# Kernel optimization log

Hardware: AMD Instinct MI355X
Metric: run time of the kernel (lower is better)

## Reference

```python
import jax, jax.numpy as jnp
import numpy as np

DIM = 768
H = 16
HD = DIM // H  # 48


def setup_inputs() -> dict:
    key = jax.random.key(0)
    ks = jax.random.split(key, 9)
    s = 0.02
    return {
        "x": jax.random.normal(ks[0], (8, 1024, DIM), dtype=jnp.float32),
        "w_qkv": jax.random.normal(ks[1], (3 * DIM, DIM), dtype=jnp.float32) * s,
        "b_qkv": jax.random.normal(ks[2], (3 * DIM,), dtype=jnp.float32) * s,
        "w_l": jax.random.normal(ks[3], (H, H), dtype=jnp.float32) * 0.25,
        "b_l": jax.random.normal(ks[4], (H,), dtype=jnp.float32) * s,
        "w_w": jax.random.normal(ks[5], (H, H), dtype=jnp.float32) * 0.25,
        "b_w": jax.random.normal(ks[6], (H,), dtype=jnp.float32) * s,
        "w_proj": jax.random.normal(ks[7], (DIM, DIM), dtype=jnp.float32) * s,
        "b_proj": jax.random.normal(ks[8], (DIM,), dtype=jnp.float32) * s,
    }


def reference(x, w_qkv, b_qkv, w_l, b_l, w_w, b_w, w_proj, b_proj):
    B, N, C = x.shape
    scale = HD ** -0.5
    qkv = x @ w_qkv.T + b_qkv                        # [B,N,3C]
    qkv = qkv.reshape(B, N, 3, H, HD).transpose(2, 0, 3, 1, 4)  # [3,B,H,N,HD]
    q = qkv[0] * scale
    k = qkv[1]
    v = qkv[2]
    attn = jnp.einsum('bhqd,bhkd->bhqk', q, k)       # [B,H,N,N]
    # talking-heads mix before softmax (Linear over head dim)
    attn = jnp.einsum('bhqk,gh->bgqk', attn, w_l) + b_l[None, :, None, None]
    attn = jax.nn.softmax(attn, axis=-1)
    # talking-heads mix after softmax
    attn = jnp.einsum('bhqk,gh->bgqk', attn, w_w) + b_w[None, :, None, None]
    out = jnp.einsum('bhqk,bhkd->bhqd', attn, v)     # [B,H,N,HD]
    out = out.transpose(0, 2, 1, 3).reshape(B, N, C)
    return out @ w_proj.T + b_proj
```

## Files before the change

kernel.cpp:

```cpp
#include <hip/hip_runtime.h>

typedef unsigned short u16;
typedef unsigned int u32;
using short8 = __attribute__((__ext_vector_type__(8))) short;
using f32x4  = __attribute__((__ext_vector_type__(4))) float;

#define DIM 768
#define QKV3 2304
#define SEQ 1024
#define SCALE 0.14433756729740643f

__device__ __forceinline__ u16 f2bf(float f) {
  __bf16 h = (__bf16)f;
  u16 r;
  __builtin_memcpy(&r, &h, 2);
  return r;
}
__device__ __forceinline__ u32 packbf(float lo, float hi) {
  return (u32)f2bf(lo) | ((u32)f2bf(hi) << 16);
}
__device__ __forceinline__ void store1(u16* p, float v) { *p = f2bf(v); }
__device__ __forceinline__ void store1(float* p, float v) { *p = v; }

__device__ __forceinline__ f32x4 mfma16(short8 a, short8 b, f32x4 c) {
  return __builtin_amdgcn_mfma_f32_16x16x32_bf16(a, b, c, 0, 0, 0);
}

__device__ __forceinline__ void gload16(const void* g, void* l) {
  __builtin_amdgcn_global_load_lds(
      (const __attribute__((address_space(1))) unsigned int*)g,
      (__attribute__((address_space(3))) unsigned int*)l, 16, 0, 0);
}

__global__ __launch_bounds__(256)
void cvt_f32_bf16(const float* __restrict__ src, u16* __restrict__ dst, int n8) {
  int i = blockIdx.x * 256 + threadIdx.x;
  if (i < n8) {
    float4 a = ((const float4*)src)[2 * i];
    float4 b = ((const float4*)src)[2 * i + 1];
    uint4 o = {packbf(a.x, a.y), packbf(a.z, a.w), packbf(b.x, b.y), packbf(b.z, b.w)};
    ((uint4*)dst)[i] = o;
  }
}

template <typename TO>
__global__ __launch_bounds__(256, 4)
void gemm_bb(const u16* __restrict__ A, const u16* __restrict__ W,
             const float* __restrict__ bias, TO* __restrict__ C,
             int M, int N, int K) {
  __shared__ __align__(16) u16 As[128 * 32];
  __shared__ __align__(16) u16 Bs[128 * 32];
  const int tid = threadIdx.x;
  const int lane = tid & 63;
  const int wv = tid >> 6;
  const int lq = lane & 15;
  const int lc = lane >> 4;
  const int wm = wv >> 1, wn = wv & 1;
  const int row0 = blockIdx.y * 128, col0 = blockIdx.x * 128;

  f32x4 acc[4][4];
#pragma unroll
  for (int i = 0; i < 4; ++i)
#pragma unroll
    for (int j = 0; j < 4; ++j) acc[i][j] = (f32x4){0.f, 0.f, 0.f, 0.f};

#pragma unroll 1
  for (int k0 = 0; k0 < K; k0 += 32) {
    __syncthreads();
#pragma unroll
    for (int i = 0; i < 2; ++i) {
      int c = i * 256 + tid;
      int r = c >> 2, kc = (c & 3) * 8;
      gload16(A + (size_t)(row0 + r) * K + k0 + kc, As + c * 8);
      gload16(W + (size_t)(col0 + r) * K + k0 + kc, Bs + c * 8);
    }
    __syncthreads();
    short8 af[4], bf8[4];
#pragma unroll
    for (int i = 0; i < 4; ++i)
      af[i] = *(const short8*)(As + (wm * 64 + i * 16 + lq) * 32 + lc * 8);
#pragma unroll
    for (int j = 0; j < 4; ++j)
      bf8[j] = *(const short8*)(Bs + (wn * 64 + j * 16 + lq) * 32 + lc * 8);
#pragma unroll
    for (int i = 0; i < 4; ++i)
#pragma unroll
      for (int j = 0; j < 4; ++j)
        acc[i][j] = mfma16(af[i], bf8[j], acc[i][j]);
  }
#pragma unroll
  for (int j = 0; j < 4; ++j) {
    int col = col0 + wn * 64 + j * 16 + lq;
    float bv = bias[col];
#pragma unroll
    for (int i = 0; i < 4; ++i)
#pragma unroll
      for (int r = 0; r < 4; ++r) {
        int row = row0 + wm * 64 + i * 16 + lc * 4 + r;
        store1(C + (size_t)row * N + col, acc[i][j][r] + bv);
      }
  }
}

#define KS_ELEMS 24848
#define SMEM_ELEMS 80416
#define ATTN_SMEM 160832

__global__ __launch_bounds__(512, 2)
void attn_kernel(const u16* __restrict__ qkv,
                 const float* __restrict__ wl, const float* __restrict__ bl,
                 const float* __restrict__ ww, const float* __restrict__ bw,
                 u16* __restrict__ obuf) {
  extern __shared__ __align__(16) u16 smem[];
  u16* const Ks0 = smem;
  u16* const Sb  = smem + KS_ELEMS;
  u16* const Vs  = smem + 2 * KS_ELEMS;

  const int tid = threadIdx.x;
  const int wv = tid >> 6;
  const int lane = tid & 63;
  const int lq = lane & 15;
  const int lc = lane >> 4;
  const int b = blockIdx.x >> 5;
  const int qt = blockIdx.x & 31;
  const size_t tokQ = (size_t)b * SEQ + (size_t)qt * 32;
  const size_t tokB = (size_t)b * SEQ;
  const int h0 = wv * 2;
  const short8 z8 = {0, 0, 0, 0, 0, 0, 0, 0};

  {
    u32* z = (u32*)smem;
    for (int i = tid; i < SMEM_ELEMS / 2; i += 512) z[i] = 0u;
  }

  short8 qf[2][2][2];
#pragma unroll
  for (int hh = 0; hh < 2; ++hh)
#pragma unroll
    for (int qs = 0; qs < 2; ++qs) {
      const u16* qp = qkv + (tokQ + qs * 16 + lq) * QKV3 + (h0 + hh) * 48;
      qf[hh][qs][0] = *(const short8*)(qp + lc * 8);
      short8 zq = z8;
      if (lc < 2) zq = *(const short8*)(qp + 32 + lc * 8);
      qf[hh][qs][1] = zq;
    }

  short8 wlF = z8;
  short8 wwF = z8;
  if (lc < 2) {
#pragma unroll
    for (int e = 0; e < 8; ++e) {
      wlF[e] = (short)f2bf(wl[lq * 16 + lc * 8 + e] * SCALE);
      wwF[e] = (short)f2bf(ww[lq * 16 + lc * 8 + e]);
    }
  }
  float blr[4];
#pragma unroll
  for (int r = 0; r < 4; ++r) blr[r] = bl[lc * 4 + r];
  const float bwq = bw[lq];

  short8 kpre[6], vA[3], vB[3];
  auto issueK = [&](int kt) {
#pragma unroll
    for (int t = 0; t < 6; ++t) {
      int j = t * 512 + tid;
      int kr = j / 96, cc = j - kr * 96;
      kpre[t] = *(const short8*)(qkv + (tokB + (size_t)kt * 32 + kr) * QKV3 + DIM + cc * 8);
    }
  };
  auto issueV = [&](int kt) {
#pragma unroll
    for (int t = 0; t < 3; ++t) {
      int cc = (tid >> 4) + t * 32;
      int kk = tid & 15;
      const u16* v0 = qkv + (tokB + (size_t)kt * 32 + 2 * kk) * QKV3 + 2 * DIM + cc * 8;
      vA[t] = *(const short8*)v0;
      vB[t] = *(const short8*)(v0 + QKV3);
    }
  };
  auto writeK = [&](u16* dst) {
#pragma unroll
    for (int t = 0; t < 6; ++t) {
      int j = t * 512 + tid;
      int kr = j / 96, cc = j - kr * 96;
      *(short8*)(dst + kr * 776 + cc * 8) = kpre[t];
    }
  };
  auto writeV = [&]() {
#pragma unroll
    for (int t = 0; t < 3; ++t) {
      int cc = (tid >> 4) + t * 32;
      int kk = tid & 15;
#pragma unroll
      for (int e = 0; e < 8; ++e)
        *(u32*)(Vs + (cc * 8 + e) * 40 + 2 * kk) =
            (u32)(u16)vA[t][e] | ((u32)(u16)vB[t][e] << 16);
    }
  };
  auto doQK = [&](const u16* kbase) {
#pragma unroll
    for (int ks = 0; ks < 2; ++ks) {
      short8 kf[2][2];
#pragma unroll
      for (int hh = 0; hh < 2; ++hh) {
        const u16* kb = kbase + (ks * 16 + lq) * 776 + (h0 + hh) * 48;
        kf[hh][0] = *(const short8*)(kb + lc * 8);
        short8 k1 = z8;
        if (lc < 2) k1 = *(const short8*)(kb + 32 + lc * 8);
        kf[hh][1] = k1;
      }
#pragma unroll
      for (int qs = 0; qs < 2; ++qs) {
        f32x4 s0 = {0.f, 0.f, 0.f, 0.f}, s1 = {0.f, 0.f, 0.f, 0.f};
        s0 = mfma16(qf[0][qs][0], kf[0][0], s0);
        s0 = mfma16(qf[0][qs][1], kf[0][1], s0);
        s1 = mfma16(qf[1][qs][0], kf[1][0], s1);
        s1 = mfma16(qf[1][qs][1], kf[1][1], s1);
#pragma unroll
        for (int r = 0; r < 4; ++r) {
          int q = qs * 16 + lc * 4 + r;
          int k = ks * 16 + lq;
          *(u32*)(Sb + q * 776 + k * 24 + h0) = packbf(s0[r], s1[r]);
        }
      }
    }
  };
  auto doPV = [&](f32x4 O[2][3][2]) {
#pragma unroll
    for (int hh = 0; hh < 2; ++hh) {
      const int g2 = h0 + hh;
      short8 w2f[2];
#pragma unroll
      for (int qs = 0; qs < 2; ++qs)
        w2f[qs] = *(const short8*)(Sb + (qs * 16 + lq) * 776 + g2 * 40 + lc * 8);
#pragma unroll
      for (int dt = 0; dt < 3; ++dt) {
        short8 vf = *(const short8*)(Vs + (g2 * 48 + dt * 16 + lq) * 40 + lc * 8);
#pragma unroll
        for (int qs = 0; qs < 2; ++qs)
          O[hh][dt][qs] = mfma16(w2f[qs], vf, O[hh][dt][qs]);
      }
    }
  };

  float Zac[4][4], invZ[4][4];
#pragma unroll
  for (int i = 0; i < 4; ++i)
#pragma unroll
    for (int r = 0; r < 4; ++r) Zac[i][r] = 0.f;

  f32x4 O[2][3][2];
#pragma unroll
  for (int hh = 0; hh < 2; ++hh)
#pragma unroll
    for (int dt = 0; dt < 3; ++dt)
#pragma unroll
      for (int qs = 0; qs < 2; ++qs) O[hh][dt][qs] = (f32x4){0.f, 0.f, 0.f, 0.f};

  issueK(0);
  __syncthreads();
  writeK(Ks0);
  issueK(1);
  __syncthreads();
#pragma unroll 1
  for (int kt = 0; kt < 32; ++kt) {
    u16* cur = (kt & 1) ? Vs : Ks0;
    u16* nxt = (kt & 1) ? Ks0 : Vs;
    if (kt < 31) {
      writeK(nxt);
      issueK(kt == 30 ? 0 : kt + 2);
    }
    doQK(cur);
    __syncthreads();
#pragma unroll
    for (int i = 0; i < 4; ++i) {
      const int q = wv * 4 + i;
      const u16* sq = Sb + q * 776;
#pragma unroll
      for (int ks = 0; ks < 2; ++ks) {
        short8 sf = z8;
        if (lc < 2) sf = *(const short8*)(sq + (ks * 16 + lq) * 24 + lc * 8);
        f32x4 cin = {blr[0], blr[1], blr[2], blr[3]};
        f32x4 L = mfma16(wlF, sf, cin);
#pragma unroll
        for (int r = 0; r < 4; ++r) Zac[i][r] += __expf(L[r]);
      }
    }
    __syncthreads();
  }
  issueV(0);
#pragma unroll
  for (int i = 0; i < 4; ++i)
#pragma unroll
    for (int r = 0; r < 4; ++r) {
      float z = Zac[i][r];
      z += __shfl_xor(z, 1);
      z += __shfl_xor(z, 2);
      z += __shfl_xor(z, 4);
      z += __shfl_xor(z, 8);
      invZ[i][r] = 1.0f / z;
    }

#pragma unroll 1
  for (int kt = 0; kt < 32; ++kt) {
    if (kt) doPV(O);
    writeK(Ks0);
    __syncthreads();
    writeV();
    doQK(Ks0);
    if (kt < 31) { issueK(kt + 1); issueV(kt + 1); }
    __syncthreads();
#pragma unroll
    for (int i = 0; i < 4; ++i) {
      const int q = wv * 4 + i;
      u16* const sq = Sb + q * 776;
      f32x4 L[2];
#pragma unroll
      for (int ks = 0; ks < 2; ++ks) {
        short8 sf = z8;
        if (lc < 2) sf = *(const short8*)(sq + (ks * 16 + lq) * 24 + lc * 8);
        f32x4 cin = {blr[0], blr[1], blr[2], blr[3]};
        L[ks] = mfma16(wlF, sf, cin);
      }
#pragma unroll
      for (int ks = 0; ks < 2; ++ks) {
        float p0 = __expf(L[ks][0]) * invZ[i][0];
        float p1 = __expf(L[ks][1]) * invZ[i][1];
        float p2 = __expf(L[ks][2]) * invZ[i][2];
        float p3 = __expf(L[ks][3]) * invZ[i][3];
        uint2 pv = {packbf(p0, p1), packbf(p2, p3)};
        *(uint2*)(sq + (ks * 16 + lq) * 24 + lc * 4) = pv;
      }
      f32x4 W2[2];
      f32x4 cw = {bwq, bwq, bwq, bwq};
#pragma unroll
      for (int ks = 0; ks < 2; ++ks) {
        short8 pf = z8;
        if (lc < 2) pf = *(const short8*)(sq + (ks * 16 + lq) * 24 + lc * 8);
        W2[ks] = mfma16(pf, wwF, cw);
      }
#pragma unroll
      for (int ks = 0; ks < 2; ++ks) {
        uint2 wv2 = {packbf(W2[ks][0], W2[ks][1]), packbf(W2[ks][2], W2[ks][3])};
        *(uint2*)(sq + lq * 40 + ks * 16 + lc * 4) = wv2;
      }
    }
    __syncthreads();
  }
  doPV(O);

#pragma unroll
  for (int hh = 0; hh < 2; ++hh)
#pragma unroll
    for (int dt = 0; dt < 3; ++dt)
#pragma unroll
      for (int qs = 0; qs < 2; ++qs)
#pragma unroll
        for (int r = 0; r < 4; ++r) {
          size_t row = tokQ + qs * 16 + lc * 4 + r;
          int col = (h0 + hh) * 48 + dt * 16 + lq;
          obuf[row * DIM + col] = f2bf(O[hh][dt][qs][r]);
        }
}

extern "C" void kernel_launch(void* const* d_in, const int* in_sizes, int n_in,
                              void* d_out, int out_size, void* d_ws, size_t ws_size,
                              hipStream_t stream) {
  const float* x      = (const float*)d_in[0];
  const float* w_qkv  = (const float*)d_in[1];
  const float* b_qkv  = (const float*)d_in[2];
  const float* w_l    = (const float*)d_in[3];
  const float* b_l    = (const float*)d_in[4];
  const float* w_w    = (const float*)d_in[5];
  const float* b_w    = (const float*)d_in[6];
  const float* w_proj = (const float*)d_in[7];
  const float* b_proj = (const float*)d_in[8];
  float* out = (float*)d_out;

  u16* qkv_buf  = (u16*)d_ws;
  u16* attn_buf = qkv_buf + (size_t)8192 * QKV3;
  u16* x_bf     = attn_buf;
  u16* w_qkv_bf  = (u16*)d_out;
  u16* w_proj_bf = qkv_buf;

  static int attr_done = 0;
  if (!attr_done) {
    (void)hipFuncSetAttribute(reinterpret_cast<const void*>(attn_kernel),
                              hipFuncAttributeMaxDynamicSharedMemorySize,
                              ATTN_SMEM);
    attr_done = 1;
  }

  cvt_f32_bf16<<<dim3(864), 256, 0, stream>>>(w_qkv, w_qkv_bf, 221184);
  cvt_f32_bf16<<<dim3(3072), 256, 0, stream>>>(x, x_bf, 786432);
  gemm_bb<u16><<<dim3(QKV3 / 128, 8192 / 128), 256, 0, stream>>>(
      x_bf, w_qkv_bf, b_qkv, qkv_buf, 8192, QKV3, DIM);
  attn_kernel<<<dim3(8 * 32), dim3(512), ATTN_SMEM, stream>>>(
      qkv_buf, w_l, b_l, w_w, b_w, attn_buf);
  cvt_f32_bf16<<<dim3(288), 256, 0, stream>>>(w_proj, w_proj_bf, 73728);
  gemm_bb<float><<<dim3(DIM / 128, 8192 / 128), 256, 0, stream>>>(
      attn_buf, w_proj_bf, b_proj, out, 8192, DIM, DIM);
}
```

Measured before the change: 382.4 us.

## Deepen GEMM K-tile to 64 with XOR-swizzled LDS and vectorize attention stores

The GEMM kernel now stages 64-wide K slices instead of 32, halving the number of loop iterations and barriers, and stores the tiles in LDS with an XOR swizzle to reduce bank conflicts on fragment reads. In the attention kernel, the conditional zero-masked LDS loads are replaced by unconditional loads that rely on zeroed padding or zero weight fragments. The PV MFMA operands are swapped, giving a transposed accumulator layout so the output can be written as packed 8-byte stores instead of scalar bf16 stores. The larger LDS tiles raise shared memory per block, which could lower occupancy for the GEMM.

```diff
diff --git a/kernel.cpp b/kernel.cpp
--- a/kernel.cpp
+++ b/kernel.cpp
@@ -48,8 +48,8 @@
 void gemm_bb(const u16* __restrict__ A, const u16* __restrict__ W,
              const float* __restrict__ bias, TO* __restrict__ C,
              int M, int N, int K) {
-  __shared__ __align__(16) u16 As[128 * 32];
-  __shared__ __align__(16) u16 Bs[128 * 32];
+  __shared__ __align__(16) u16 As[128 * 64];
+  __shared__ __align__(16) u16 Bs[128 * 64];
   const int tid = threadIdx.x;
   const int lane = tid & 63;
   const int wv = tid >> 6;
@@ -65,28 +65,36 @@
     for (int j = 0; j < 4; ++j) acc[i][j] = (f32x4){0.f, 0.f, 0.f, 0.f};
 
 #pragma unroll 1
-  for (int k0 = 0; k0 < K; k0 += 32) {
-    __syncthreads();
-#pragma unroll
-    for (int i = 0; i < 2; ++i) {
+  for (int k0 = 0; k0 < K; k0 += 64) {
+    __syncthreads();
+#pragma unroll
+    for (int i = 0; i < 4; ++i) {
       int c = i * 256 + tid;
-      int r = c >> 2, kc = (c & 3) * 8;
+      int r = c >> 3;
+      int kc = ((c & 7) ^ (r & 7)) * 8;
       gload16(A + (size_t)(row0 + r) * K + k0 + kc, As + c * 8);
       gload16(W + (size_t)(col0 + r) * K + k0 + kc, Bs + c * 8);
     }
     __syncthreads();
-    short8 af[4], bf8[4];
-#pragma unroll
-    for (int i = 0; i < 4; ++i)
-      af[i] = *(const short8*)(As + (wm * 64 + i * 16 + lq) * 32 + lc * 8);
-#pragma unroll
-    for (int j = 0; j < 4; ++j)
-      bf8[j] = *(const short8*)(Bs + (wn * 64 + j * 16 + lq) * 32 + lc * 8);
-#pragma unroll
-    for (int i = 0; i < 4; ++i)
-#pragma unroll
-      for (int j = 0; j < 4; ++j)
-        acc[i][j] = mfma16(af[i], bf8[j], acc[i][j]);
+#pragma unroll
+    for (int kk = 0; kk < 2; ++kk) {
+      short8 af[4], bf8[4];
+#pragma unroll
+      for (int i = 0; i < 4; ++i) {
+        int R = wm * 64 + i * 16 + lq;
+        af[i] = *(const short8*)(As + R * 64 + (((kk * 4 + lc) ^ (R & 7)) * 8));
+      }
+#pragma unroll
+      for (int j = 0; j < 4; ++j) {
+        int R = wn * 64 + j * 16 + lq;
+        bf8[j] = *(const short8*)(Bs + R * 64 + (((kk * 4 + lc) ^ (R & 7)) * 8));
+      }
+#pragma unroll
+      for (int i = 0; i < 4; ++i)
+#pragma unroll
+        for (int j = 0; j < 4; ++j)
+          acc[i][j] = mfma16(af[i], bf8[j], acc[i][j]);
+    }
   }
 #pragma unroll
   for (int j = 0; j < 4; ++j) {
@@ -126,7 +134,6 @@
   const size_t tokQ = (size_t)b * SEQ + (size_t)qt * 32;
   const size_t tokB = (size_t)b * SEQ;
   const int h0 = wv * 2;
-  const short8 z8 = {0, 0, 0, 0, 0, 0, 0, 0};
 
   {
     u32* z = (u32*)smem;
@@ -140,13 +147,13 @@
     for (int qs = 0; qs < 2; ++qs) {
       const u16* qp = qkv + (tokQ + qs * 16 + lq) * QKV3 + (h0 + hh) * 48;
       qf[hh][qs][0] = *(const short8*)(qp + lc * 8);
-      short8 zq = z8;
+      short8 zq = {0, 0, 0, 0, 0, 0, 0, 0};
       if (lc < 2) zq = *(const short8*)(qp + 32 + lc * 8);
       qf[hh][qs][1] = zq;
     }
 
-  short8 wlF = z8;
-  short8 wwF = z8;
+  short8 wlF = {0, 0, 0, 0, 0, 0, 0, 0};
+  short8 wwF = {0, 0, 0, 0, 0, 0, 0, 0};
   if (lc < 2) {
 #pragma unroll
     for (int e = 0; e < 8; ++e) {
@@ -205,9 +212,7 @@
       for (int hh = 0; hh < 2; ++hh) {
         const u16* kb = kbase + (ks * 16 + lq) * 776 + (h0 + hh) * 48;
         kf[hh][0] = *(const short8*)(kb + lc * 8);
-        short8 k1 = z8;
-        if (lc < 2) k1 = *(const short8*)(kb + 32 + lc * 8);
-        kf[hh][1] = k1;
+        kf[hh][1] = *(const short8*)(kb + 32 + lc * 8);
       }
 #pragma unroll
       for (int qs = 0; qs < 2; ++qs) {
@@ -238,7 +243,7 @@
         short8 vf = *(const short8*)(Vs + (g2 * 48 + dt * 16 + lq) * 40 + lc * 8);
 #pragma unroll
         for (int qs = 0; qs < 2; ++qs)
-          O[hh][dt][qs] = mfma16(w2f[qs], vf, O[hh][dt][qs]);
+          O[hh][dt][qs] = mfma16(vf, w2f[qs], O[hh][dt][qs]);
       }
     }
   };
@@ -278,8 +283,7 @@
       const u16* sq = Sb + q * 776;
 #pragma unroll
       for (int ks = 0; ks < 2; ++ks) {
-        short8 sf = z8;
-        if (lc < 2) sf = *(const short8*)(sq + (ks * 16 + lq) * 24 + lc * 8);
+        short8 sf = *(const short8*)(sq + (ks * 16 + lq) * 24 + lc * 8);
         f32x4 cin = {blr[0], blr[1], blr[2], blr[3]};
         f32x4 L = mfma16(wlF, sf, cin);
 #pragma unroll
@@ -317,8 +321,7 @@
       f32x4 L[2];
 #pragma unroll
       for (int ks = 0; ks < 2; ++ks) {
-        short8 sf = z8;
-        if (lc < 2) sf = *(const short8*)(sq + (ks * 16 + lq) * 24 + lc * 8);
+        short8 sf = *(const short8*)(sq + (ks * 16 + lq) * 24 + lc * 8);
         f32x4 cin = {blr[0], blr[1], blr[2], blr[3]};
         L[ks] = mfma16(wlF, sf, cin);
       }
@@ -335,8 +338,7 @@
       f32x4 cw = {bwq, bwq, bwq, bwq};
 #pragma unroll
       for (int ks = 0; ks < 2; ++ks) {
-        short8 pf = z8;
-        if (lc < 2) pf = *(const short8*)(sq + (ks * 16 + lq) * 24 + lc * 8);
+        short8 pf = *(const short8*)(sq + (ks * 16 + lq) * 24 + lc * 8);
         W2[ks] = mfma16(pf, wwF, cw);
       }
 #pragma unroll
@@ -354,13 +356,13 @@
 #pragma unroll
     for (int dt = 0; dt < 3; ++dt)
 #pragma unroll
-      for (int qs = 0; qs < 2; ++qs)
-#pragma unroll
-        for (int r = 0; r < 4; ++r) {
-          size_t row = tokQ + qs * 16 + lc * 4 + r;
-          int col = (h0 + hh) * 48 + dt * 16 + lq;
-          obuf[row * DIM + col] = f2bf(O[hh][dt][qs][r]);
-        }
+      for (int qs = 0; qs < 2; ++qs) {
+        size_t row = tokQ + qs * 16 + lq;
+        int col = (h0 + hh) * 48 + dt * 16 + lc * 4;
+        uint2 p = {packbf(O[hh][dt][qs][0], O[hh][dt][qs][1]),
+                   packbf(O[hh][dt][qs][2], O[hh][dt][qs][3])};
+        *(uint2*)(obuf + row * DIM + col) = p;
+      }
 }
 
 extern "C" void kernel_launch(void* const* d_in, const int* in_sizes, int n_in,
```

New measurement: 356.6 us. 1.07x faster.
